# Kernel tuning notes

Hardware: AMD Instinct MI355X
Metric: run time of the kernel (lower is better)

The kernel has to match this reference:

```python
import math
import jax, jax.numpy as jnp
import numpy as np


def setup_inputs() -> dict:
    key = jax.random.key(0)
    kq, kk, kv = jax.random.split(key, 3)
    bs, n_tok, n_heads, width = 2, 2048, 8, 64
    deg = 32  # neighbors per dst token -> coo_cnt_max
    q = jax.random.normal(kq, (bs, n_tok, n_heads, width), dtype=jnp.float32)
    k = jax.random.normal(kk, (bs, n_tok, n_heads, width), dtype=jnp.float32)
    v = jax.random.normal(kv, (bs, n_tok, n_heads, width), dtype=jnp.float32)
    rng = np.random.default_rng(0)
    dst = np.repeat(np.arange(n_tok), deg)            # [cl]
    src = rng.integers(0, n_tok, size=n_tok * deg)    # [cl]
    sm = np.tile(np.arange(deg), n_tok)               # [cl], unique per dst
    coo = jnp.asarray(np.stack([dst, src, sm], axis=1), dtype=jnp.int32)  # [cl,3]
    return {"q": q, "k": k, "v": v, "coo": coo, "coo_cnt_max": deg}


def reference(q, k, v, coo, coo_cnt_max):
    bs, n_tok, n_heads, width = q.shape
    dst, src, sm = coo[:, 0], coo[:, 1], coo[:, 2]
    # [b, h, t, w] layout
    qq = q.transpose(0, 2, 1, 3)
    kk = k.transpose(0, 2, 1, 3)
    vv = v.transpose(0, 2, 1, 3)
    scale = -1.0 / math.sqrt(width)
    # per-edge negative scaled L1 distance: [b, h, cl]
    ww = jnp.sum(jnp.abs(qq[:, :, dst, :] - kk[:, :, src, :]), axis=-1) * scale
    neg_big = jnp.asarray(-1e32, dtype=q.dtype)
    # scatter edge scores into dense padded attention slots: [b, h, t, cnt+1]
    attn = jnp.full((bs, n_heads, n_tok, coo_cnt_max + 1), neg_big, dtype=q.dtype)
    attn = attn.at[:, :, dst, sm].set(ww)
    attn_sm = jax.nn.softmax(attn, axis=-1)
    # scatter values into padded neighbor-value tensor: [b, h, t, cnt+1, w]
    vw = jnp.zeros((bs, n_heads, n_tok, coo_cnt_max + 1, width), dtype=q.dtype)
    vw = vw.at[:, :, dst, sm, :].set(vv[:, :, src, :])
    vo = jnp.einsum('bhds,bhdsw->bdhw', attn_sm, vw)
    # only dst tokens appearing in coo receive output; others stay zero
    vout = jnp.zeros_like(v).at[:, dst, :, :].set(vo[:, dst, :, :])
    return vout
```

## Files before the change

### kernel.cpp

```cpp
#include <hip/hip_runtime.h>
#include <hip/hip_bf16.h>

#define BS   2
#define NT   2048
#define NH   8
#define WD   64
#define DEG  32

#define PK_ROWS   (BS * 4 * NT)
#define PK_ROW_B  512
#define PK_UINTS  (PK_ROWS * (PK_ROW_B / 4))

typedef _Float16 half2_t __attribute__((ext_vector_type(2)));

#if defined(__has_builtin)
#if __has_builtin(__builtin_amdgcn_fdot2)
#define HAVE_FDOT2 1
#endif
#endif

__device__ __forceinline__ unsigned short f2h(float f) {
    _Float16 h = (_Float16)f;
    unsigned short u; __builtin_memcpy(&u, &h, 2); return u;
}
__device__ __forceinline__ half2_t u2h2(unsigned int w) {
    half2_t r; __builtin_memcpy(&r, &w, 4); return r;
}
__device__ __forceinline__ unsigned int h22u(half2_t h) {
    unsigned int u; __builtin_memcpy(&u, &h, 4); return u;
}
__device__ __forceinline__ half2_t habs2(half2_t x) {
    unsigned int u = h22u(x) & 0x7fff7fffu;
    return u2h2(u);
}

__global__ __launch_bounds__(256) void pack_kv_f16(
    const float* __restrict__ k,
    const float* __restrict__ v,
    unsigned int* __restrict__ packed)
{
    const int u    = blockIdx.x * 256 + threadIdx.x;
    const int row  = u >> 7;
    const int pos  = u & 127;
    const int part = pos >> 6;
    const int e    = pos & 63;
    const int s    = row & (NT - 1);
    const int hp   = (row >> 11) & 3;
    const int b    = row >> 13;
    const int elem = e * 2;
    const int h_in = elem >> 6;
    const int w0   = elem & 63;

    const float* src = (part == 0 ? k : v)
        + (((size_t)(b * NT + s) * NH + hp * 2 + h_in) << 6) + w0;
    float2 f = *(const float2*)src;
    packed[u] = (unsigned int)f2h(f.x) | ((unsigned int)f2h(f.y) << 16);
}

__global__ __launch_bounds__(64) void l1attn_main_f16(
    const float* __restrict__ q,
    const unsigned int* __restrict__ packed,
    const int* __restrict__ coo,
    float* __restrict__ out)
{
    const int bid   = blockIdx.x;
    const int combo = bid & 7;
    const int hp    = combo & 3;
    const int b     = combo >> 2;
    const int t     = bid >> 3;
    const int ln    = threadIdx.x;
    const int hw    = ln >> 5;
    const int l     = ln & 31;

    __shared__ int          s_src[DEG];
    __shared__ unsigned int s_q[64];
    __shared__ unsigned int s_k[DEG * 64];

    if (ln < DEG) {
        s_src[ln] = coo[(t * DEG + ln) * 3 + 1];
    }
    {
        const float2* qrow = (const float2*)
            (q + ((size_t)(b * NT + t) * NH + hp * 2) * WD);
        float2 qv = qrow[ln];
        s_q[ln] = (unsigned int)f2h(qv.x) | ((unsigned int)f2h(qv.y) << 16);
    }
    __syncthreads();

    const size_t combo_base = (size_t)((b * 4 + hp) * NT) * (PK_ROW_B / 4);

    {
        const int rsub = ln >> 4;
        const int c    = ln & 15;
        #pragma unroll
        for (int r = 0; r < 8; ++r) {
            const int j = 4 * r + rsub;
            const int s = s_src[j];
            const int chunk = (c + j) & 15;
            const char* gaddr = (const char*)(packed + combo_base)
                              + (size_t)s * PK_ROW_B + chunk * 16;
            char* laddr = (char*)s_k + 4 * r * 256;
            __builtin_amdgcn_global_load_lds(
                (const __attribute__((address_space(1))) void*)gaddr,
                (__attribute__((address_space(3))) void*)laddr,
                16, 0, 0);
        }
    }

    const int jg = l >> 4;
    const int wq = l & 15;
    uint2 vr[16];
    {
        const char* vbase = (const char*)(packed + combo_base)
                          + (16 + hw * 8) * 16 + wq * 8;
        #pragma unroll
        for (int i = 0; i < 16; ++i) {
            const int sv = s_src[2 * i + jg];
            vr[i] = *(const uint2*)(vbase + (size_t)sv * PK_ROW_B);
        }
    }

    asm volatile("s_waitcnt vmcnt(16)" ::: "memory");

    float acc = 0.f;
#ifdef HAVE_FDOT2
    const half2_t one2 = {(_Float16)1.0f, (_Float16)1.0f};
#endif
    #pragma unroll
    for (int i = 0; i < 8; ++i) {
        const int slot = ((hw * 8 + i) - l) & 15;
        uint4 c = *(const uint4*)((const char*)s_k + l * 256 + slot * 16);
        const unsigned int ws[4] = {c.x, c.y, c.z, c.w};
        #pragma unroll
        for (int m = 0; m < 4; ++m) {
            half2_t kh = u2h2(ws[m]);
            half2_t qh = u2h2(s_q[hw * 32 + i * 4 + m]);
            half2_t ad = habs2(qh - kh);
#ifdef HAVE_FDOT2
            acc = __builtin_amdgcn_fdot2(ad, one2, acc, false);
#else
            acc += (float)ad.x + (float)ad.y;
#endif
        }
    }
    float logit = -0.125f * acc;

    float m = logit;
    #pragma unroll
    for (int d = 16; d >= 1; d >>= 1) m = fmaxf(m, __shfl_xor(m, d));
    float e = __expf(logit - m);
    float ssum = e;
    #pragma unroll
    for (int d = 16; d >= 1; d >>= 1) ssum += __shfl_xor(ssum, d);
    const float p = e / ssum;

    int p2i;
    {
        _Float16 ph = (_Float16)p;
        half2_t p2 = {ph, ph};
        p2i = h22u(p2);
    }
    half2_t a0 = {(_Float16)0.0f, (_Float16)0.0f};
    half2_t a1 = a0;
    #pragma unroll
    for (int i = 0; i < 16; ++i) {
        const int pj2i = __shfl(p2i, 2 * i + jg, 32);
        half2_t pj2 = u2h2(pj2i);
        a0 = __builtin_elementwise_fma(pj2, u2h2(vr[i].x), a0);
        a1 = __builtin_elementwise_fma(pj2, u2h2(vr[i].y), a1);
    }
    {
        unsigned int u0 = h22u(a0), u1 = h22u(a1);
        unsigned int o0 = __shfl_xor((int)u0, 16);
        unsigned int o1 = __shfl_xor((int)u1, 16);
        a0 = a0 + u2h2(o0);
        a1 = a1 + u2h2(o1);
    }

    if (jg == 0) {
        const int h = hp * 2 + hw;
        float4 res = make_float4((float)a0.x, (float)a0.y,
                                 (float)a1.x, (float)a1.y);
        *(float4*)(out + ((size_t)(b * NT + t) * NH + h) * WD + 4 * wq) = res;
    }
}

__global__ __launch_bounds__(64) void l1attn_sparse_fp32(
    const float* __restrict__ q,
    const float* __restrict__ k,
    const float* __restrict__ v,
    const int* __restrict__ coo,
    float* __restrict__ out)
{
    const int bid   = blockIdx.x;
    const int combo = bid & 7;
    const int hp    = combo & 3;
    const int b     = combo >> 2;
    const int t     = bid >> 3;
    const int ln    = threadIdx.x;
    const int hw    = ln >> 5;
    const int l     = ln & 31;

    __shared__ int   s_src[DEG];
    __shared__ float s_q[2 * WD];
    __shared__ float s_k[DEG * 2 * WD];

    if (ln < DEG) s_src[ln] = coo[(t * DEG + ln) * 3 + 1];
    {
        const float2* qrow = (const float2*)
            (q + ((size_t)(b * NT + t) * NH + hp * 2) * WD);
        float2 qv = qrow[ln];
        s_q[2 * ln] = qv.x; s_q[2 * ln + 1] = qv.y;
    }
    __syncthreads();
    {
        #pragma unroll
        for (int r = 0; r < 16; ++r) {
            const int j = 2 * r + hw;
            const int s = s_src[j];
            const int chunk = (l + j) & 31;
            const float* gaddr = k + ((size_t)(b * NT + s) * NH + hp * 2) * WD
                               + chunk * 4;
            float* laddr = s_k + 2 * r * (2 * WD);
            __builtin_amdgcn_global_load_lds(
                (const __attribute__((address_space(1))) void*)gaddr,
                (__attribute__((address_space(3))) void*)laddr, 16, 0, 0);
        }
    }
    const int h  = hp * 2 + hw;
    const int jg = l >> 4;
    const int wq = l & 15;
    float4 vr[16];
    #pragma unroll
    for (int i = 0; i < 16; ++i) {
        const int sv = s_src[2 * i + jg];
        vr[i] = *(const float4*)(v + ((size_t)(b * NT + sv) * NH + h) * WD + 4 * wq);
    }
    __syncthreads();
    const float* qh = s_q + hw * WD;
    float acc = 0.f;
    #pragma unroll
    for (int i = 0; i < 16; ++i) {
        const int slot = ((hw * 16 + i) - l) & 31;
        float4 kv = *(const float4*)(s_k + l * (2 * WD) + slot * 4);
        const int wb = i * 4;
        acc += fabsf(qh[wb] - kv.x) + fabsf(qh[wb + 1] - kv.y)
             + fabsf(qh[wb + 2] - kv.z) + fabsf(qh[wb + 3] - kv.w);
    }
    float logit = -0.125f * acc;
    float m = logit;
    #pragma unroll
    for (int d = 16; d >= 1; d >>= 1) m = fmaxf(m, __shfl_xor(m, d));
    float e = __expf(logit - m);
    float ssum = e;
    #pragma unroll
    for (int d = 16; d >= 1; d >>= 1) ssum += __shfl_xor(ssum, d);
    const float p = e / ssum;
    float4 o4 = make_float4(0.f, 0.f, 0.f, 0.f);
    #pragma unroll
    for (int i = 0; i < 16; ++i) {
        const float pj = __shfl(p, 2 * i + jg, 32);
        o4.x += pj * vr[i].x; o4.y += pj * vr[i].y;
        o4.z += pj * vr[i].z; o4.w += pj * vr[i].w;
    }
    o4.x += __shfl_xor(o4.x, 16); o4.y += __shfl_xor(o4.y, 16);
    o4.z += __shfl_xor(o4.z, 16); o4.w += __shfl_xor(o4.w, 16);
    if (jg == 0)
        *(float4*)(out + ((size_t)(b * NT + t) * NH + h) * WD + 4 * wq) = o4;
}

extern "C" void kernel_launch(void* const* d_in, const int* in_sizes, int n_in,
                              void* d_out, int out_size, void* d_ws, size_t ws_size,
                              hipStream_t stream) {
    const float* q   = (const float*)d_in[0];
    const float* k   = (const float*)d_in[1];
    const float* v   = (const float*)d_in[2];
    const int*   coo = (const int*)d_in[3];
    float*       o   = (float*)d_out;

    if (ws_size >= (size_t)PK_UINTS * 4) {
        unsigned int* packed = (unsigned int*)d_ws;
        hipLaunchKernelGGL(pack_kv_f16, dim3(PK_UINTS / 256), dim3(256), 0,
                           stream, k, v, packed);
        hipLaunchKernelGGL(l1attn_main_f16, dim3(BS * NT * 4), dim3(64), 0,
                           stream, q, packed, coo, o);
    } else {
        hipLaunchKernelGGL(l1attn_sparse_fp32, dim3(BS * NT * 4), dim3(64), 0,
                           stream, q, k, v, coo, o);
    }
}
```

Before: 98.01 us.

## Split K-row loads between LDS DMA and direct register loads

```diff
diff --git a/kernel.cpp b/kernel.cpp
--- a/kernel.cpp
+++ b/kernel.cpp
@@ -6,6 +6,7 @@
 #define NH   8
 #define WD   64
 #define DEG  32
+#define NDMA 24
 
 #define PK_ROWS   (BS * 4 * NT)
 #define PK_ROW_B  512
@@ -32,6 +33,15 @@
 __device__ __forceinline__ half2_t habs2(half2_t x) {
     unsigned int u = h22u(x) & 0x7fff7fffu;
     return u2h2(u);
+}
+__device__ __forceinline__ float l1_half2(float acc, half2_t qh, half2_t kh) {
+    half2_t ad = habs2(qh - kh);
+#ifdef HAVE_FDOT2
+    const half2_t one2 = {(_Float16)1.0f, (_Float16)1.0f};
+    return __builtin_amdgcn_fdot2(ad, one2, acc, false);
+#else
+    return acc + (float)ad.x + (float)ad.y;
+#endif
 }
 
 __global__ __launch_bounds__(256) void pack_kv_f16(
@@ -88,17 +98,17 @@
     __syncthreads();
 
     const size_t combo_base = (size_t)((b * 4 + hp) * NT) * (PK_ROW_B / 4);
+    const char*  cbase      = (const char*)(packed + combo_base);
 
     {
         const int rsub = ln >> 4;
         const int c    = ln & 15;
         #pragma unroll
-        for (int r = 0; r < 8; ++r) {
+        for (int r = 0; r < NDMA / 4; ++r) {
             const int j = 4 * r + rsub;
             const int s = s_src[j];
             const int chunk = (c + j) & 15;
-            const char* gaddr = (const char*)(packed + combo_base)
-                              + (size_t)s * PK_ROW_B + chunk * 16;
+            const char* gaddr = cbase + (size_t)s * PK_ROW_B + chunk * 16;
             char* laddr = (char*)s_k + 4 * r * 256;
             __builtin_amdgcn_global_load_lds(
                 (const __attribute__((address_space(1))) void*)gaddr,
@@ -109,10 +119,20 @@
 
     const int jg = l >> 4;
     const int wq = l & 15;
+
+    uint2 kr[4];
+    {
+        const char* kbase = cbase + hw * 128 + wq * 8;
+        #pragma unroll
+        for (int i = 0; i < 4; ++i) {
+            const int sv = s_src[2 * (12 + i) + jg];
+            kr[i] = *(const uint2*)(kbase + (size_t)sv * PK_ROW_B);
+        }
+    }
+
     uint2 vr[16];
     {
-        const char* vbase = (const char*)(packed + combo_base)
-                          + (16 + hw * 8) * 16 + wq * 8;
+        const char* vbase = cbase + (16 + hw * 8) * 16 + wq * 8;
         #pragma unroll
         for (int i = 0; i < 16; ++i) {
             const int sv = s_src[2 * i + jg];
@@ -120,12 +140,37 @@
         }
     }
 
-    asm volatile("s_waitcnt vmcnt(16)" ::: "memory");
+    asm volatile("s_waitcnt vmcnt(20)" ::: "memory");
+
+    float racc[4] = {0.f, 0.f, 0.f, 0.f};
+    {
+        half2_t q0 = u2h2(s_q[hw * 32 + wq * 2]);
+        half2_t q1 = u2h2(s_q[hw * 32 + wq * 2 + 1]);
+        #pragma unroll
+        for (int i = 0; i < 4; ++i) {
+            racc[i] = l1_half2(racc[i], q0, u2h2(kr[i].x));
+            racc[i] = l1_half2(racc[i], q1, u2h2(kr[i].y));
+        }
+    }
+    #pragma unroll
+    for (int d = 8; d >= 1; d >>= 1) {
+        #pragma unroll
+        for (int i = 0; i < 4; ++i) racc[i] += __shfl_xor(racc[i], d);
+    }
+    float rlog;
+    {
+        const int srcl = (l & 1) * 16;
+        float c0 = __shfl(racc[0], srcl, 32);
+        float c1 = __shfl(racc[1], srcl, 32);
+        float c2 = __shfl(racc[2], srcl, 32);
+        float c3 = __shfl(racc[3], srcl, 32);
+        const int idx = (l >> 1) - 12;
+        float lo = (idx & 1) ? c1 : c0;
+        float hi = (idx & 1) ? c3 : c2;
+        rlog = (idx & 2) ? hi : lo;
+    }
 
     float acc = 0.f;
-#ifdef HAVE_FDOT2
-    const half2_t one2 = {(_Float16)1.0f, (_Float16)1.0f};
-#endif
     #pragma unroll
     for (int i = 0; i < 8; ++i) {
         const int slot = ((hw * 8 + i) - l) & 15;
@@ -133,17 +178,11 @@
         const unsigned int ws[4] = {c.x, c.y, c.z, c.w};
         #pragma unroll
         for (int m = 0; m < 4; ++m) {
-            half2_t kh = u2h2(ws[m]);
-            half2_t qh = u2h2(s_q[hw * 32 + i * 4 + m]);
-            half2_t ad = habs2(qh - kh);
-#ifdef HAVE_FDOT2
-            acc = __builtin_amdgcn_fdot2(ad, one2, acc, false);
-#else
-            acc += (float)ad.x + (float)ad.y;
-#endif
-        }
-    }
-    float logit = -0.125f * acc;
+            acc = l1_half2(acc, u2h2(s_q[hw * 32 + i * 4 + m]), u2h2(ws[m]));
+        }
+    }
+    float dist  = (l >= NDMA) ? rlog : acc;
+    float logit = -0.125f * dist;
 
     float m = logit;
     #pragma unroll
@@ -170,9 +209,8 @@
         a1 = __builtin_elementwise_fma(pj2, u2h2(vr[i].y), a1);
     }
     {
-        unsigned int u0 = h22u(a0), u1 = h22u(a1);
-        unsigned int o0 = __shfl_xor((int)u0, 16);
-        unsigned int o1 = __shfl_xor((int)u1, 16);
+        unsigned int o0 = __shfl_xor((int)h22u(a0), 16);
+        unsigned int o1 = __shfl_xor((int)h22u(a1), 16);
         a0 = a0 + u2h2(o0);
         a1 = a1 + u2h2(o1);
     }
```

New measurement: 98.92 us. About the same (+0.9%).
